# Optimization experiments

Hardware: AMD Instinct MI355X
Metric: run time of the kernel (lower is better)

Reference implementation:

```python
import jax, jax.numpy as jnp
import numpy as np
import math

EMBED_DIM = 512
NUM_HEADS = 8
NUM_EXPERTS = 16
TOP_K = 8
B, T = 2, 1024


def setup_inputs() -> dict:
    key = jax.random.key(0)
    ks = jax.random.split(key, 16)
    d, E = EMBED_DIM, NUM_EXPERTS
    hdim = 4 * d  # expert hidden width
    s = 0.02
    inp = {
        "x": jax.random.normal(ks[0], (B, T, d), jnp.float32),
        # RMSNorm params (init ones, matching torch module)
        "g": jnp.ones((d,), jnp.float32),
        "b": jnp.ones((d,), jnp.float32),
        # attention
        "c_attn_w": jax.random.normal(ks[1], (d, 3 * d), jnp.float32) * s,
        "c_attn_b": jnp.zeros((3 * d,), jnp.float32),
        "alpha": jnp.ones((NUM_HEADS,), jnp.float32),
        "c_proj_w": jax.random.normal(ks[2], (d, d), jnp.float32) * s,
        "c_proj_b": jnp.zeros((d,), jnp.float32),
        # router
        "router_w": jax.random.normal(ks[3], (d, E), jnp.float32) * s,
        "router_b": jnp.zeros((E,), jnp.float32),
        # stacked expert params: Linear(d,4d) -> SwiGLU(4d,4d) -> Linear(4d,d)
        "w_in": jax.random.normal(ks[4], (E, d, hdim), jnp.float32) * s,
        "b_in": jnp.zeros((E, hdim), jnp.float32),
        "w1": jax.random.normal(ks[5], (E, hdim, 2 * hdim), jnp.float32) * s,
        "b1": jnp.zeros((E, 2 * hdim), jnp.float32),
        "w2": jax.random.normal(ks[6], (E, hdim, hdim), jnp.float32) * s,
        "b2": jnp.zeros((E, hdim), jnp.float32),
        "w_out": jax.random.normal(ks[7], (E, hdim, d), jnp.float32) * s,
        "b_out": jnp.zeros((E, d), jnp.float32),
    }
    return inp


def _block(x, g, b, c_attn_w, c_attn_b, alpha, c_proj_w, c_proj_b,
           router_w, router_b, w_in, b_in, w1, b1, w2, b2, w_out, b_out):
    Bb, Tt, C = x.shape
    H = alpha.shape[0]
    hd = C // H
    E = router_b.shape[0]

    # RMSNorm (note: additive b, per original module)
    rms = jnp.sqrt(jnp.mean(x * x, axis=-1, keepdims=True) + 1e-6)
    xn = (x / rms) * g + b

    # QK-normalized causal attention
    qkv = xn @ c_attn_w + c_attn_b                      # [B,T,3C]
    q, k, v = jnp.split(qkv, 3, axis=-1)
    def heads(t):
        return t.reshape(Bb, Tt, H, hd).transpose(0, 2, 1, 3)  # [B,H,T,hd]
    q, k, v = heads(q), heads(k), heads(v)
    eps = 1e-5
    q_hat = q / (jnp.linalg.norm(q, axis=-1, keepdims=True) + eps)
    k_hat = k / (jnp.linalg.norm(k, axis=-1, keepdims=True) + eps)
    factor = (alpha * math.sqrt(hd)).reshape(1, H, 1, 1)
    q_scaled = q_hat * factor
    # SDPA default scale = 1/sqrt(head_dim)
    scores = jnp.einsum("bhqd,bhkd->bhqk", q_scaled, k_hat) / math.sqrt(hd)
    causal = jnp.tril(jnp.ones((Tt, Tt), bool))
    scores = jnp.where(causal, scores, -jnp.inf)
    att = jax.nn.softmax(scores, axis=-1)
    y = jnp.einsum("bhqk,bhkd->bhqd", att, v)
    y = y.transpose(0, 2, 1, 3).reshape(Bb, Tt, C)
    y = y @ c_proj_w + c_proj_b
    x = x + y

    # Router + top-8 normalized gates
    routes = jax.nn.softmax(x @ router_w + router_b, axis=-1)  # [B,T,E]
    probs, idx = jax.lax.top_k(routes, TOP_K)
    probs = probs / jnp.sum(probs, axis=-1, keepdims=True)
    # combine weights per expert: [B,T,E]
    gates = jnp.sum(jax.nn.one_hot(idx, E, dtype=x.dtype) * probs[..., None], axis=2)

    # Dense expert evaluation (faithful math: unselected tokens get zero gate)
    N = Bb * Tt
    xf = x.reshape(N, C)
    gf = gates.reshape(N, E)
    h = jnp.einsum("nd,edf->enf", xf, w_in) + b_in[:, None, :]      # [E,N,4d]
    c = jnp.einsum("enf,efg->eng", h, w1) + b1[:, None, :]          # [E,N,8d]
    a, bb2 = jnp.split(c, 2, axis=-1)
    s = (bb2 * jax.nn.sigmoid(bb2)) * a                              # SwiGLU
    o = jnp.einsum("enf,efg->eng", s, w2) + b2[:, None, :]          # [E,N,4d]
    eo = jnp.einsum("enf,efd->end", o, w_out) + b_out[:, None, :]   # [E,N,d]
    moe = jnp.einsum("end,ne->nd", eo, gf).reshape(Bb, Tt, C)
    return x + moe


def reference(x, g, b, c_attn_w, c_attn_b, alpha, c_proj_w, c_proj_b,
              router_w, router_b, w_in, b_in, w1, b1, w2, b2, w_out, b_out):
    return _block(x, g, b, c_attn_w, c_attn_b, alpha, c_proj_w, c_proj_b,
                  router_w, router_b, w_in, b_in, w1, b1, w2, b2, w_out, b_out)
```

## Files before the change

### kernel.cpp

```cpp
#include <hip/hip_runtime.h>
#include <stdint.h>

#define DEVI __device__ __forceinline__
#define FENCE() asm volatile("" ::: "memory")
#define BAR() do{ FENCE(); __builtin_amdgcn_s_barrier(); FENCE(); }while(0)

typedef short short8 __attribute__((ext_vector_type(8)));
typedef short short4v __attribute__((ext_vector_type(4)));
typedef float f32x4 __attribute__((ext_vector_type(4)));

DEVI float bf2f(unsigned short s){ union{unsigned u; float f;} x; x.u = ((unsigned)s)<<16; return x.f; }
DEVI unsigned short f2bf(float f){ union{float f; unsigned u;} x; x.f=f; unsigned r = x.u + 0x7fff + ((x.u>>16)&1); return (unsigned short)(r>>16); }

DEVI void gload_lds16(const void* g, void* l){
  __builtin_amdgcn_global_load_lds((const __attribute__((address_space(1))) unsigned int*)g,
                                   (__attribute__((address_space(3))) unsigned int*)l, 16, 0, 0);
}

__global__ __launch_bounds__(256)
void prep_all(const float* __restrict__ caw, const float* __restrict__ cpw,
              const float* __restrict__ w_in, const float* __restrict__ w1,
              const float* __restrict__ w2, const float* __restrict__ w_out,
              unsigned short* __restrict__ wT_attn, unsigned short* __restrict__ wT_proj,
              unsigned short* __restrict__ wT_in, unsigned short* __restrict__ wT1p,
              unsigned short* __restrict__ wT_2, unsigned short* __restrict__ wT_out,
              const float* __restrict__ x, const float* __restrict__ gw,
              const float* __restrict__ bw, unsigned short* __restrict__ xn)
{
  __shared__ float tile[8][32][33];
  int bid = blockIdx.x;
  int t = threadIdx.x;
  int tr = t>>3, tc = (t&7)*4;

  const float* src = nullptr; unsigned short* dst = nullptr;
  int K=0, N=0, kb=0, nb0=0;

  if (bid < 96){
    int xb8 = bid % 6, yb = bid / 6;
    src = caw; dst = wT_attn; K=512; N=1536; kb=yb*32; nb0=xb8*256;
  } else if ((bid -= 96) < 32){
    int xb8 = bid % 2, yb = bid / 2;
    src = cpw; dst = wT_proj; K=512; N=512; kb=yb*32; nb0=xb8*256;
  } else if ((bid -= 32) < 2048){
    int z = bid >> 7, r = bid & 127;
    int xb8 = r % 8, yb = r / 8;
    src = w_in + (size_t)z*512*2048; dst = wT_in + (size_t)z*2048*512;
    K=512; N=2048; kb=yb*32; nb0=xb8*256;
  } else if ((bid -= 2048) < 16384){
    int z = bid >> 10, r = bid & 1023;
    int xb8 = r % 16, yb = r / 16;
    const float* s1 = w1 + (size_t)z*2048*4096;
    unsigned short* d1 = wT1p + (size_t)z*4096*2048;
    int k0 = yb*32;
    float4 v[8];
    #pragma unroll
    for (int j=0;j<8;j++){
      int g = xb8*8 + j;
      int srccol = (tc < 16) ? (g*16 + tc) : (2048 + g*16 + (tc-16));
      v[j] = *(const float4*)(s1 + (size_t)(k0+tr)*4096 + srccol);
    }
    #pragma unroll
    for (int j=0;j<8;j++){
      tile[j][tr][tc+0]=v[j].x; tile[j][tr][tc+1]=v[j].y;
      tile[j][tr][tc+2]=v[j].z; tile[j][tr][tc+3]=v[j].w;
    }
    __syncthreads();
    #pragma unroll
    for (int j=0;j<8;j++){
      int np0 = xb8*256 + 32*j;
      short4v ov;
      ov[0] = (short)f2bf(tile[j][tc+0][tr]);
      ov[1] = (short)f2bf(tile[j][tc+1][tr]);
      ov[2] = (short)f2bf(tile[j][tc+2][tr]);
      ov[3] = (short)f2bf(tile[j][tc+3][tr]);
      *(short4v*)(d1 + (size_t)(np0+tr)*2048 + k0 + tc) = ov;
    }
    return;
  } else if ((bid -= 16384) < 8192){
    int z = bid >> 9, r = bid & 511;
    int xb8 = r % 8, yb = r / 8;
    src = w2 + (size_t)z*2048*2048; dst = wT_2 + (size_t)z*2048*2048;
    K=2048; N=2048; kb=yb*32; nb0=xb8*256;
  } else if ((bid -= 8192) < 2048){
    int z = bid >> 7, r = bid & 127;
    int xb8 = r % 2, yb = r / 2;
    src = w_out + (size_t)z*2048*512; dst = wT_out + (size_t)z*512*2048;
    K=2048; N=512; kb=yb*32; nb0=xb8*256;
  } else {
    bid -= 2048;
    int row = bid*4 + (t>>6);
    int lane = t & 63;
    const float* xr = x + (size_t)row*512 + lane*8;
    float4 a = *(const float4*)xr;
    float4 c = *(const float4*)(xr+4);
    float ss = a.x*a.x+a.y*a.y+a.z*a.z+a.w*a.w + c.x*c.x+c.y*c.y+c.z*c.z+c.w*c.w;
    #pragma unroll
    for (int m=1;m<64;m<<=1) ss += __shfl_xor(ss, m);
    float inv = 1.0f / sqrtf(ss*(1.f/512.f) + 1e-6f);
    const float* gr = gw + lane*8; const float* br = bw + lane*8;
    float4 g0=*(const float4*)gr, g1=*(const float4*)(gr+4);
    float4 b0=*(const float4*)br, b1=*(const float4*)(br+4);
    short8 o;
    o[0]=(short)f2bf(a.x*inv*g0.x + b0.x);
    o[1]=(short)f2bf(a.y*inv*g0.y + b0.y);
    o[2]=(short)f2bf(a.z*inv*g0.z + b0.z);
    o[3]=(short)f2bf(a.w*inv*g0.w + b0.w);
    o[4]=(short)f2bf(c.x*inv*g1.x + b1.x);
    o[5]=(short)f2bf(c.y*inv*g1.y + b1.y);
    o[6]=(short)f2bf(c.z*inv*g1.z + b1.z);
    o[7]=(short)f2bf(c.w*inv*g1.w + b1.w);
    *(short8*)(xn + (size_t)row*512 + lane*8) = o;
    return;
  }
  {
    float4 v[8];
    #pragma unroll
    for (int j=0;j<8;j++)
      v[j] = *(const float4*)(src + (size_t)(kb+tr)*N + nb0 + 32*j + tc);
    #pragma unroll
    for (int j=0;j<8;j++){
      tile[j][tr][tc+0]=v[j].x; tile[j][tr][tc+1]=v[j].y;
      tile[j][tr][tc+2]=v[j].z; tile[j][tr][tc+3]=v[j].w;
    }
    __syncthreads();
    #pragma unroll
    for (int j=0;j<8;j++){
      short4v ov;
      ov[0] = (short)f2bf(tile[j][tc+0][tr]);
      ov[1] = (short)f2bf(tile[j][tc+1][tr]);
      ov[2] = (short)f2bf(tile[j][tc+2][tr]);
      ov[3] = (short)f2bf(tile[j][tc+3][tr]);
      *(short4v*)(dst + (size_t)(nb0+32*j+tr)*K + kb + tc) = ov;
    }
  }
}

#define READ_AFR(Q) do{ \
  _Pragma("unroll") \
  for (int m2=0;m2<2;m2++){ \
    int rt = wm*128 + ((Q)*2+m2)*16 + lrow; \
    _Pragma("unroll") \
    for (int kk=0;kk<2;kk++) \
      afr[m2][kk] = *(const short8*)(sA + rt*128 + (((lg+kk*4)^(rt&7))<<4)); \
  } \
}while(0)

#define QUADP(Q) do{ \
  __builtin_amdgcn_s_setprio(1); \
  _Pragma("unroll") \
  for (int m2=0;m2<2;m2++){ \
    _Pragma("unroll") \
    for (int n=0;n<4;n++){ \
      _Pragma("unroll") \
      for (int kk=0;kk<2;kk++) \
        acc[(Q)*2+m2][n] = __builtin_amdgcn_mfma_f32_16x16x32_bf16(afr[m2][kk], bfr[n][kk], acc[(Q)*2+m2][n], 0,0,0); \
    } \
  } \
  __builtin_amdgcn_s_setprio(0); \
}while(0)

template<int EPI>
__global__ __launch_bounds__(512, 2)
void gemmT(const unsigned short* __restrict__ A, const unsigned short* __restrict__ B,
           const float* __restrict__ bias,
           unsigned short* __restrict__ Ch,
           int M, int N, int K,
           const int* __restrict__ off, long long strideBz, long long strideBiasz)
{
  __shared__ char smem[131072];
  int z = blockIdx.z;
  int rowbase = 0, Mz = M;
  if (off){ rowbase = off[z]; Mz = off[z+1] - rowbase; }
  int row0 = blockIdx.y * 256;
  if (row0 >= Mz) return;
  int col0 = blockIdx.x * 256;
  const unsigned short* Ab = A + (size_t)(rowbase + row0) * K;
  const unsigned short* Bb = B + (size_t)z * strideBz + (size_t)col0 * K;
  const float* biasz = bias + (size_t)z * strideBiasz;

  int tid = threadIdx.x;
  int lane = tid & 63, w = tid >> 6;
  int lrow = lane & 15, lg = lane >> 4;
  int wm = w >> 2, wn = w & 3;

  f32x4 acc[8][4];
  #pragma unroll
  for (int i=0;i<8;i++){
    #pragma unroll
    for (int j=0;j<4;j++) acc[i][j] = f32x4{0.f,0.f,0.f,0.f};
  }
  int nkt = K >> 6;
  auto stage = [&](int kt2, int H){
    if (kt2 >= nkt) return;
    char* sl = smem + (kt2 & 1) * 65536 + H * 16384;
    int k0 = kt2 << 6;
    const unsigned short* src = (H < 2) ? Ab : Bb;
    int rbase = (H & 1) * 128;
    #pragma unroll
    for (int i=0;i<2;i++){
      int si = i*512 + tid;
      int r = si >> 3, kb = (si & 7) ^ (r & 7);
      gload_lds16(src + (size_t)(rbase + r)*K + k0 + kb*8, sl + si*16);
    }
  };
  stage(0,0); stage(0,1); stage(0,2); stage(0,3);
  stage(1,2); stage(1,3);
  asm volatile("s_waitcnt vmcnt(4)" ::: "memory");
  BAR();
  for (int kt = 0; kt < nkt; kt++){
    char* sA = smem + (kt & 1) * 65536;
    char* sB = sA + 32768;
    short8 bfr[4][2], afr[2][2];
    #pragma unroll
    for (int n=0;n<4;n++){
      int ct = wn*64 + n*16 + lrow;
      #pragma unroll
      for (int kk=0;kk<2;kk++)
        bfr[n][kk] = *(const short8*)(sB + ct*128 + (((lg+kk*4)^(ct&7))<<4));
    }
    READ_AFR(0);
    stage(kt+1, 0); stage(kt+1, 1);
    BAR();
    QUADP(0);
    BAR();
    READ_AFR(1);
    stage(kt+2, 2);
    BAR();
    QUADP(1);
    BAR();
    READ_AFR(2);
    stage(kt+2, 3);
    BAR();
    QUADP(2);
    BAR();
    READ_AFR(3);
    if (kt + 2 < nkt) { asm volatile("s_waitcnt vmcnt(4)" ::: "memory"); }
    else              { asm volatile("s_waitcnt vmcnt(0)" ::: "memory"); }
    BAR();
    QUADP(3);
    BAR();
  }
  #pragma unroll
  for (int m=0;m<8;m++){
    #pragma unroll
    for (int j=0;j<4;j++){
      int row = row0 + wm*128 + m*16 + lg*4 + j;
      if (row < Mz){
        size_t rg = (size_t)(rowbase + row);
        if constexpr (EPI == 2){
          #pragma unroll
          for (int nf=0;nf<4;nf+=2){
            int pcol = col0 + wn*64 + nf*16;
            int scol = ((pcol>>5)<<4) + lrow;
            float av = acc[m][nf][j]   + biasz[scol];
            float gv = acc[m][nf+1][j] + biasz[2048 + scol];
            float sg = gv / (1.f + __expf(-gv));
            Ch[rg*2048 + scol] = f2bf(av * sg);
          }
        } else {
          #pragma unroll
          for (int n=0;n<4;n++){
            int col = col0 + wn*64 + n*16 + lrow;
            float v = acc[m][n][j] + biasz[col];
            Ch[rg * N + col] = f2bf(v);
          }
        }
      }
    }
  }
}

__global__ __launch_bounds__(256)
void gemm_qkv(const unsigned short* __restrict__ A, const unsigned short* __restrict__ B,
              const float* __restrict__ bias, const float* __restrict__ alpha,
              unsigned short* __restrict__ oq, unsigned short* __restrict__ ok,
              unsigned short* __restrict__ ov, int N, int K)
{
  __shared__ char smem[32768];
  char* smA = smem; char* smB = smem + 16384;
  int row0 = blockIdx.y * 128;
  int col0 = blockIdx.x * 128;
  int t = threadIdx.x, w = t>>6, lane = t&63;
  int lrow = lane&15, lg = lane>>4;
  int wr = w>>1, wc = w&1;

  f32x4 acc[4][4];
  #pragma unroll
  for (int i=0;i<4;i++){
    #pragma unroll
    for (int j=0;j<4;j++) acc[i][j] = f32x4{0.f,0.f,0.f,0.f};
  }
  const size_t Abase = (size_t)row0 * K;
  const size_t Bbase = (size_t)col0 * K;
  int nkt = K >> 6;
  for (int kt=0; kt<nkt; kt++){
    __syncthreads();
    int k0 = kt*64;
    #pragma unroll
    for (int i=0;i<4;i++){
      int s = (i*4 + w)*64 + lane;
      int r = s>>3;
      int kb = (s&7) ^ (r&7);
      gload_lds16(A + Abase + (size_t)r*K + k0 + kb*8, smA + (size_t)(i*4+w)*1024);
      gload_lds16(B + Bbase + (size_t)r*K + k0 + kb*8, smB + (size_t)(i*4+w)*1024);
    }
    __syncthreads();
    #pragma unroll
    for (int ks=0; ks<2; ks++){
      short8 af[4], bf[4];
      int kbb = lg + ks*4;
      #pragma unroll
      for (int m=0;m<4;m++){
        int rt = wr*64 + m*16 + lrow;
        af[m] = *(const short8*)(smA + rt*128 + ((kbb ^ (rt&7))<<4));
      }
      #pragma unroll
      for (int n=0;n<4;n++){
        int rt = wc*64 + n*16 + lrow;
        bf[n] = *(const short8*)(smB + rt*128 + ((kbb ^ (rt&7))<<4));
      }
      #pragma unroll
      for (int m=0;m<4;m++){
        #pragma unroll
        for (int n=0;n<4;n++)
          acc[m][n] = __builtin_amdgcn_mfma_f32_16x16x32_bf16(af[m], bf[n], acc[m][n], 0,0,0);
      }
    }
  }
  int tcol = col0 + wc*64;
  int type = tcol >> 9;
  int hd = (tcol >> 6) & 7;
  float al = alpha[hd];
  #pragma unroll
  for (int m=0;m<4;m++){
    #pragma unroll
    for (int j=0;j<4;j++){
      int row = row0 + wr*64 + m*16 + lg*4 + j;
      float v4[4]; float ss = 0.f;
      #pragma unroll
      for (int n=0;n<4;n++){
        v4[n] = acc[m][n][j] + bias[tcol + n*16 + lrow];
        ss += v4[n]*v4[n];
      }
      ss += __shfl_xor(ss,1); ss += __shfl_xor(ss,2);
      ss += __shfl_xor(ss,4); ss += __shfl_xor(ss,8);
      int b = row >> 10, tt = row & 1023;
      size_t hb = ((size_t)(b*8+hd))*65536;
      if (type == 0){
        float sc = al / (sqrtf(ss) + 1e-5f);
        #pragma unroll
        for (int n=0;n<4;n++)
          oq[hb + (size_t)tt*64 + n*16 + lrow] = f2bf(v4[n]*sc);
      } else if (type == 1){
        float sc = 1.f / (sqrtf(ss) + 1e-5f);
        #pragma unroll
        for (int n=0;n<4;n++)
          ok[hb + (size_t)tt*64 + n*16 + lrow] = f2bf(v4[n]*sc);
      } else {
        #pragma unroll
        for (int n=0;n<4;n++)
          ov[((size_t)(b*8+hd)*64 + n*16 + lrow)*1024 + tt] = f2bf(v4[n]);
      }
    }
  }
}

__global__ __launch_bounds__(256)
void gemm_proj(const unsigned short* __restrict__ A, const unsigned short* __restrict__ B,
               const float* __restrict__ bias,
               float* __restrict__ Cf, unsigned short* __restrict__ Ch,
               const float* __restrict__ resid, int M, int N, int K)
{
  __shared__ char smem[32768];
  char* smA = smem; char* smB = smem + 16384;
  int row0 = blockIdx.y * 128;
  int col0 = blockIdx.x * 128;
  int t = threadIdx.x, w = t>>6, lane = t&63;
  int lrow = lane&15, lg = lane>>4;
  int wr = w>>1, wc = w&1;

  f32x4 acc[4][4];
  #pragma unroll
  for (int i=0;i<4;i++){
    #pragma unroll
    for (int j=0;j<4;j++) acc[i][j] = f32x4{0.f,0.f,0.f,0.f};
  }
  const size_t Abase = (size_t)row0 * K;
  const size_t Bbase = (size_t)col0 * K;
  int nkt = K >> 6;
  for (int kt=0; kt<nkt; kt++){
    __syncthreads();
    int k0 = kt*64;
    #pragma unroll
    for (int i=0;i<4;i++){
      int s = (i*4 + w)*64 + lane;
      int r = s>>3;
      int kb = (s&7) ^ (r&7);
      gload_lds16(A + Abase + (size_t)r*K + k0 + kb*8, smA + (size_t)(i*4+w)*1024);
      gload_lds16(B + Bbase + (size_t)r*K + k0 + kb*8, smB + (size_t)(i*4+w)*1024);
    }
    __syncthreads();
    #pragma unroll
    for (int ks=0; ks<2; ks++){
      short8 af[4], bf[4];
      int kbb = lg + ks*4;
      #pragma unroll
      for (int m=0;m<4;m++){
        int rt = wr*64 + m*16 + lrow;
        af[m] = *(const short8*)(smA + rt*128 + ((kbb ^ (rt&7))<<4));
      }
      #pragma unroll
      for (int n=0;n<4;n++){
        int rt = wc*64 + n*16 + lrow;
        bf[n] = *(const short8*)(smB + rt*128 + ((kbb ^ (rt&7))<<4));
      }
      #pragma unroll
      for (int m=0;m<4;m++){
        #pragma unroll
        for (int n=0;n<4;n++)
          acc[m][n] = __builtin_amdgcn_mfma_f32_16x16x32_bf16(af[m], bf[n], acc[m][n], 0,0,0);
      }
    }
  }
  #pragma unroll
  for (int m=0;m<4;m++){
    int rloc = wr*64 + m*16 + lg*4;
    #pragma unroll
    for (int j=0;j<4;j++){
      int row = row0 + rloc + j;
      size_t rg = (size_t)row;
      #pragma unroll
      for (int n=0;n<4;n++){
        int col = col0 + wc*64 + n*16 + lrow;
        float v = acc[m][n][j] + bias[col];
        size_t idx = rg * N + col;
        v += resid[idx];
        Cf[idx] = v;
        Ch[idx] = f2bf(v);
      }
    }
  }
}

__global__ __launch_bounds__(256)
void attn_k(const unsigned short* __restrict__ q_s, const unsigned short* __restrict__ k_hat,
            const unsigned short* __restrict__ v_t, unsigned short* __restrict__ y)
{
  __shared__ char sm[51200];
  char* smK = sm + 18432;
  char* smV = sm + 34816;
  int qt = blockIdx.x, bh = blockIdx.y;
  int b = bh>>3, h = bh&7;
  int t = threadIdx.x, w = t>>6, lane = t&63;
  int lrow = lane&15, lg = lane>>4;
  int q0 = qt*64;
  const size_t hQK = (size_t)bh*1024*64;
  const size_t hV  = (size_t)bh*64*1024;

  #pragma unroll
  for (int i=0;i<2;i++){
    int si = i*256 + t;
    int r = si>>3, kb = (si&7)^(r&7);
    gload_lds16(q_s + hQK + (size_t)(q0+r)*64 + kb*8, sm + (size_t)si*16);
  }
  __syncthreads();
  short8 qf[2];
  #pragma unroll
  for (int ks=0;ks<2;ks++){
    int rt = w*16 + lrow;
    int kbb = lg + ks*4;
    qf[ks] = *(const short8*)(sm + rt*128 + ((kbb^(rt&7))<<4));
  }
  f32x4 oacc[4];
  #pragma unroll
  for (int j=0;j<4;j++) oacc[j] = f32x4{0.f,0.f,0.f,0.f};
  float mrun[4], lrun[4];
  #pragma unroll
  for (int j=0;j<4;j++){ mrun[j] = -1e30f; lrun[j] = 0.f; }
  char* Pw = sm + w*2304;

  int ktmax = (q0 + 63) >> 7;
  for (int kt=0; kt<=ktmax; kt++){
    __syncthreads();
    int t0 = kt*128;
    #pragma unroll
    for (int i=0;i<4;i++){
      int s = (i*4+w)*64 + lane;
      int r = s>>3, kb = (s&7)^(r&7);
      gload_lds16(k_hat + hQK + (size_t)(t0+r)*64 + kb*8, smK + (size_t)(i*4+w)*1024);
    }
    #pragma unroll
    for (int i=0;i<4;i++){
      int s = (i*4+w)*64 + lane;
      int d = s>>4, kb2 = s&15;
      int kb = kb2 ^ (d&7);
      gload_lds16(v_t + hV + (size_t)d*1024 + t0 + kb*8, smV + (size_t)(i*4+w)*1024);
    }
    __syncthreads();

    f32x4 sacc[8];
    #pragma unroll
    for (int j=0;j<8;j++) sacc[j] = f32x4{0.f,0.f,0.f,0.f};
    #pragma unroll
    for (int ks=0;ks<2;ks++){
      short8 kf[8];
      int kbb = lg + ks*4;
      #pragma unroll
      for (int nf=0;nf<8;nf++){
        int rt = nf*16+lrow;
        kf[nf] = *(const short8*)(smK + rt*128 + ((kbb^(rt&7))<<4));
      }
      #pragma unroll
      for (int nf=0;nf<8;nf++)
        sacc[nf] = __builtin_amdgcn_mfma_f32_16x16x32_bf16(qf[ks], kf[nf], sacc[nf], 0,0,0);
    }
    if (kt == ktmax){
      #pragma unroll
      for (int nf=0;nf<8;nf++){
        #pragma unroll
        for (int j=0;j<4;j++){
          int qi = q0 + w*16 + lg*4 + j;
          int ki = t0 + nf*16 + lrow;
          if (ki > qi) sacc[nf][j] = -1e30f;
        }
      }
    }
    #pragma unroll
    for (int j=0;j<4;j++){
      float mx = sacc[0][j];
      #pragma unroll
      for (int nf=1;nf<8;nf++) mx = fmaxf(mx, sacc[nf][j]);
      #pragma unroll
      for (int m=1;m<16;m<<=1) mx = fmaxf(mx, __shfl_xor(mx, m));
      float mnew = fmaxf(mrun[j], mx);
      float sc = __expf(mrun[j] - mnew);
      float rs = 0.f;
      #pragma unroll
      for (int nf=0;nf<8;nf++){
        float p = __expf(sacc[nf][j] - mnew);
        sacc[nf][j] = p; rs += p;
      }
      #pragma unroll
      for (int m=1;m<16;m<<=1) rs += __shfl_xor(rs, m);
      lrun[j] = lrun[j]*sc + rs;
      mrun[j] = mnew;
      #pragma unroll
      for (int n2=0;n2<4;n2++) oacc[n2][j] *= sc;
    }
    #pragma unroll
    for (int half=0; half<2; half++){
      #pragma unroll
      for (int nfh=0;nfh<4;nfh++){
        int nf = half*4 + nfh;
        #pragma unroll
        for (int j=0;j<4;j++){
          int row = lg*4 + j;
          int col = nfh*16 + lrow;
          *(unsigned short*)(Pw + (row*72 + col)*2) = f2bf(sacc[nf][j]);
        }
      }
      #pragma unroll
      for (int k2=0;k2<2;k2++){
        int ks2 = half*2 + k2;
        short8 pf, vf[4];
        pf = *(const short8*)(Pw + lrow*144 + lg*16 + k2*64);
        #pragma unroll
        for (int n2=0;n2<4;n2++){
          int d = n2*16+lrow;
          int kbb2 = lg + ks2*4;
          vf[n2] = *(const short8*)(smV + d*256 + ((kbb2^(d&7))<<4));
        }
        #pragma unroll
        for (int n2=0;n2<4;n2++)
          oacc[n2] = __builtin_amdgcn_mfma_f32_16x16x32_bf16(pf, vf[n2], oacc[n2], 0,0,0);
      }
    }
  }
  #pragma unroll
  for (int n2=0;n2<4;n2++){
    #pragma unroll
    for (int j=0;j<4;j++){
      float v = oacc[n2][j] / lrun[j];
      int qi = q0 + w*16 + lg*4 + j;
      int d = n2*16 + lrow;
      y[((size_t)(b*1024+qi))*512 + h*64 + d] = f2bf(v);
    }
  }
}

__global__ __launch_bounds__(256)
void router_topk(const float* __restrict__ x2f, const float* __restrict__ rw,
                 const float* __restrict__ rb, float* __restrict__ gates)
{
  int tkn = blockIdx.x*4 + (threadIdx.x>>6);
  int lane = threadIdx.x & 63;
  int e = lane & 15, p = lane >> 4;
  const float* xr = x2f + (size_t)tkn*512;
  float part = 0.f;
  for (int d = p*128; d < p*128+128; d++)
    part += xr[d] * rw[d*16 + e];
  part += __shfl_xor(part, 16);
  part += __shfl_xor(part, 32);
  float logit = part + rb[e];
  float mx = logit;
  #pragma unroll
  for (int m=1;m<16;m<<=1) mx = fmaxf(mx, __shfl_xor(mx, m));
  float ex = __expf(logit - mx);
  float sm = ex;
  #pragma unroll
  for (int m=1;m<16;m<<=1) sm += __shfl_xor(sm, m);
  float prob = ex / sm;
  bool taken = false;
  float ssum = 0.f;
  #pragma unroll
  for (int r=0;r<8;r++){
    float cv = taken ? -1.f : prob;
    int ci = e;
    #pragma unroll
    for (int m=1;m<16;m<<=1){
      float ov = __shfl_xor(cv, m);
      int oi = __shfl_xor(ci, m);
      if (ov > cv || (ov == cv && oi < ci)){ cv = ov; ci = oi; }
    }
    if (e == ci) taken = true;
    ssum += cv;
  }
  if (lane < 16)
    gates[(size_t)tkn*16 + e] = taken ? prob / ssum : 0.f;
}

__global__ void listbuild(const float* __restrict__ gates, int* __restrict__ list,
                          int* __restrict__ slot, int* __restrict__ cnt)
{
  int e = blockIdx.x;
  int tid = threadIdx.x, w = tid>>6, lane = tid&63;
  __shared__ int sbase;
  __shared__ int wsum[4];
  if (tid==0) sbase = 0;
  __syncthreads();
  for (int c=0;c<8;c++){
    int tk = c*256 + tid;
    bool flag = gates[(size_t)tk*16 + e] > 0.f;
    unsigned long long bal = __ballot(flag);
    if (lane==0) wsum[w] = (int)__popcll(bal);
    __syncthreads();
    int wpref = 0;
    for (int i=0;i<w;i++) wpref += wsum[i];
    int tot = wsum[0]+wsum[1]+wsum[2]+wsum[3];
    int lpref = (int)__popcll(bal & ((1ull<<lane)-1ull));
    if (flag){
      int pos = sbase + wpref + lpref;
      list[e*2048 + pos] = tk;
      slot[(size_t)tk*16 + e] = pos;
    }
    __syncthreads();
    if (tid==0) sbase += tot;
    __syncthreads();
  }
  if (tid==0) cnt[e] = sbase;
}

__global__ void prefix_off(const int* __restrict__ cnt, int* __restrict__ off){
  if (threadIdx.x==0 && blockIdx.x==0){
    int a=0;
    for (int e=0;e<16;e++){ off[e]=a; a+=cnt[e]; }
    off[16]=a;
  }
}

__global__ __launch_bounds__(256)
void gather_rows(const unsigned short* __restrict__ x2h, const int* __restrict__ list,
                 const int* __restrict__ cnt, const int* __restrict__ off,
                 unsigned short* __restrict__ xe)
{
  int e = blockIdx.y;
  int s = blockIdx.x*4 + (threadIdx.x>>6);
  if (s >= cnt[e]) return;
  int lane = threadIdx.x & 63;
  int tk = list[e*2048 + s];
  *(short8*)(xe + ((size_t)(off[e]+s))*512 + lane*8) =
      *(const short8*)(x2h + (size_t)tk*512 + lane*8);
}

__global__ __launch_bounds__(256)
void combine_k(const float* __restrict__ x2f, const unsigned short* __restrict__ eo,
               const float* __restrict__ gates, const int* __restrict__ slot,
               const int* __restrict__ off, float* __restrict__ out)
{
  int tkn = blockIdx.x;
  __shared__ float gs[16];
  __shared__ int rws[16];
  int tid = threadIdx.x;
  if (tid < 16){
    float g = gates[(size_t)tkn*16 + tid];
    gs[tid] = g;
    rws[tid] = (g > 0.f) ? (off[tid] + slot[(size_t)tkn*16 + tid]) : 0;
  }
  __syncthreads();
  for (int d = tid; d < 512; d += 256){
    float v = x2f[(size_t)tkn*512 + d];
    #pragma unroll
    for (int e=0;e<16;e++){
      float g = gs[e];
      if (g > 0.f) v += g * bf2f(eo[(size_t)rws[e]*512 + d]);
    }
    out[(size_t)tkn*512 + d] = v;
  }
}

extern "C" void kernel_launch(void* const* d_in, const int* in_sizes, int n_in,
                              void* d_out, int out_size, void* d_ws, size_t ws_size,
                              hipStream_t stream) {
  (void)in_sizes; (void)n_in; (void)out_size; (void)ws_size;
  const float* x    = (const float*)d_in[0];
  const float* gw   = (const float*)d_in[1];
  const float* bw   = (const float*)d_in[2];
  const float* caw  = (const float*)d_in[3];
  const float* cab  = (const float*)d_in[4];
  const float* alpha= (const float*)d_in[5];
  const float* cpw  = (const float*)d_in[6];
  const float* cpb  = (const float*)d_in[7];
  const float* rw   = (const float*)d_in[8];
  const float* rb   = (const float*)d_in[9];
  const float* w_in = (const float*)d_in[10];
  const float* b_in = (const float*)d_in[11];
  const float* w1   = (const float*)d_in[12];
  const float* b1   = (const float*)d_in[13];
  const float* w2   = (const float*)d_in[14];
  const float* b2   = (const float*)d_in[15];
  const float* w_out= (const float*)d_in[16];
  const float* b_out= (const float*)d_in[17];

  char* ws = (char*)d_ws;
  size_t o = 0;
  auto alloc = [&](size_t bytes)->char*{
    char* p = ws + o;
    o += (bytes + 255) & ~(size_t)255;
    return p;
  };
  const size_t PADROWS = 16896;
  unsigned short* wT_attn = (unsigned short*)alloc(1536ull*512*2);
  unsigned short* wT_proj = (unsigned short*)alloc(512ull*512*2);
  unsigned short* wT_in   = (unsigned short*)alloc(16ull*2048*512*2);
  unsigned short* wT1p    = (unsigned short*)alloc(16ull*4096*2048*2);
  unsigned short* wT_2    = (unsigned short*)alloc(16ull*2048*2048*2);
  unsigned short* wT_out  = (unsigned short*)alloc(16ull*512*2048*2);
  unsigned short* xn      = (unsigned short*)alloc(2048ull*512*2);
  unsigned short* q_s     = (unsigned short*)alloc(2048ull*512*2);
  unsigned short* k_hat   = (unsigned short*)alloc(2048ull*512*2);
  unsigned short* v_t     = (unsigned short*)alloc(2048ull*512*2);
  unsigned short* ybuf    = (unsigned short*)alloc(2048ull*512*2);
  float*          x2f     = (float*)alloc(2048ull*512*4);
  unsigned short* x2h     = (unsigned short*)alloc(2048ull*512*2);
  float*          gates   = (float*)alloc(2048ull*16*4);
  int*            slot    = (int*)alloc(2048ull*16*4);
  int*            list    = (int*)alloc(16ull*2048*4);
  int*            cnt     = (int*)alloc(64);
  int*            off     = (int*)alloc(256);
  unsigned short* xe      = (unsigned short*)alloc(PADROWS*512*2);
  unsigned short* hbuf    = (unsigned short*)alloc(PADROWS*2048*2);
  unsigned short* sbuf    = (unsigned short*)alloc(PADROWS*2048*2);
  unsigned short* eobuf   = xe;
  unsigned short* obuf    = hbuf;

  dim3 blk(256);
  dim3 blk5(512);
  prep_all<<<29312, blk, 0, stream>>>(caw, cpw, w_in, w1, w2, w_out,
                                      wT_attn, wT_proj, wT_in, wT1p, wT_2, wT_out,
                                      x, gw, bw, xn);

  gemm_qkv<<<dim3(12, 16), blk, 0, stream>>>(xn, wT_attn, cab, alpha,
                                             q_s, k_hat, v_t, 1536, 512);
  attn_k<<<dim3(16,16), blk, 0, stream>>>(q_s, k_hat, v_t, ybuf);
  gemm_proj<<<dim3(4,16,1), blk, 0, stream>>>(ybuf, wT_proj, cpb, x2f, x2h, x, 2048, 512, 512);
  router_topk<<<512, blk, 0, stream>>>(x2f, rw, rb, gates);
  listbuild<<<16, blk, 0, stream>>>(gates, list, slot, cnt);
  prefix_off<<<1, 64, 0, stream>>>(cnt, off);
  gather_rows<<<dim3(512,16), blk, 0, stream>>>(x2h, list, cnt, off, xe);

  gemmT<1><<<dim3(8,8,16), blk5, 0, stream>>>(xe, wT_in, b_in, hbuf,
                                              0, 2048, 512, off, 2048ll*512, 2048);
  gemmT<2><<<dim3(16,8,16), blk5, 0, stream>>>(hbuf, wT1p, b1, sbuf,
                                               0, 4096, 2048, off, 4096ll*2048, 4096);
  gemmT<1><<<dim3(8,8,16), blk5, 0, stream>>>(sbuf, wT_2, b2, obuf,
                                              0, 2048, 2048, off, 2048ll*2048, 2048);
  gemmT<1><<<dim3(2,8,16), blk5, 0, stream>>>(obuf, wT_out, b_out, eobuf,
                                              0, 512, 2048, off, 512ll*2048, 512);
  combine_k<<<2048, blk, 0, stream>>>(x2f, eobuf, gates, slot, off, (float*)d_out);
}
```

Baseline: 1.002 ms.

## Replace pipelined 256x256 expert GEMM with simple 128x128 single-buffer kernel

The expert GEMMs move from a 512-thread kernel with 256x256 tiles, double-buffered LDS and staged prefetch interleaved with MFMA quads to a 256-thread kernel with 128x128 tiles and one LDS buffer that loads then computes each k-step. Smaller tiles cut padding waste on experts with few rows and raise block count and occupancy. The cost is no global-load/compute overlap, two syncthreads per k-step, and less operand reuse per block, which increases global traffic.

Result: slower. 1.056 ms (+5.3%).

```diff
diff --git a/kernel.cpp b/kernel.cpp
--- a/kernel.cpp
+++ b/kernel.cpp
@@ -135,122 +135,81 @@
   }
 }
 
-#define READ_AFR(Q) do{ \
-  _Pragma("unroll") \
-  for (int m2=0;m2<2;m2++){ \
-    int rt = wm*128 + ((Q)*2+m2)*16 + lrow; \
-    _Pragma("unroll") \
-    for (int kk=0;kk<2;kk++) \
-      afr[m2][kk] = *(const short8*)(sA + rt*128 + (((lg+kk*4)^(rt&7))<<4)); \
-  } \
-}while(0)
-
-#define QUADP(Q) do{ \
-  __builtin_amdgcn_s_setprio(1); \
-  _Pragma("unroll") \
-  for (int m2=0;m2<2;m2++){ \
-    _Pragma("unroll") \
-    for (int n=0;n<4;n++){ \
-      _Pragma("unroll") \
-      for (int kk=0;kk<2;kk++) \
-        acc[(Q)*2+m2][n] = __builtin_amdgcn_mfma_f32_16x16x32_bf16(afr[m2][kk], bfr[n][kk], acc[(Q)*2+m2][n], 0,0,0); \
-    } \
-  } \
-  __builtin_amdgcn_s_setprio(0); \
-}while(0)
-
 template<int EPI>
-__global__ __launch_bounds__(512, 2)
-void gemmT(const unsigned short* __restrict__ A, const unsigned short* __restrict__ B,
+__global__ __launch_bounds__(256)
+void gemmE(const unsigned short* __restrict__ A, const unsigned short* __restrict__ B,
            const float* __restrict__ bias,
            unsigned short* __restrict__ Ch,
-           int M, int N, int K,
+           int N, int K,
            const int* __restrict__ off, long long strideBz, long long strideBiasz)
 {
-  __shared__ char smem[131072];
+  __shared__ char smem[32768];
+  char* smA = smem; char* smB = smem + 16384;
   int z = blockIdx.z;
-  int rowbase = 0, Mz = M;
-  if (off){ rowbase = off[z]; Mz = off[z+1] - rowbase; }
-  int row0 = blockIdx.y * 256;
+  int rowbase = off[z], Mz = off[z+1] - rowbase;
+  int row0 = blockIdx.y * 128;
   if (row0 >= Mz) return;
-  int col0 = blockIdx.x * 256;
+  int col0 = blockIdx.x * 128;
   const unsigned short* Ab = A + (size_t)(rowbase + row0) * K;
   const unsigned short* Bb = B + (size_t)z * strideBz + (size_t)col0 * K;
   const float* biasz = bias + (size_t)z * strideBiasz;
 
-  int tid = threadIdx.x;
-  int lane = tid & 63, w = tid >> 6;
-  int lrow = lane & 15, lg = lane >> 4;
-  int wm = w >> 2, wn = w & 3;
-
-  f32x4 acc[8][4];
-  #pragma unroll
-  for (int i=0;i<8;i++){
+  int t = threadIdx.x, w = t>>6, lane = t&63;
+  int lrow = lane&15, lg = lane>>4;
+  int wr = w>>1, wc = w&1;
+
+  f32x4 acc[4][4];
+  #pragma unroll
+  for (int i=0;i<4;i++){
     #pragma unroll
     for (int j=0;j<4;j++) acc[i][j] = f32x4{0.f,0.f,0.f,0.f};
   }
   int nkt = K >> 6;
-  auto stage = [&](int kt2, int H){
-    if (kt2 >= nkt) return;
-    char* sl = smem + (kt2 & 1) * 65536 + H * 16384;
-    int k0 = kt2 << 6;
-    const unsigned short* src = (H < 2) ? Ab : Bb;
-    int rbase = (H & 1) * 128;
-    #pragma unroll
-    for (int i=0;i<2;i++){
-      int si = i*512 + tid;
-      int r = si >> 3, kb = (si & 7) ^ (r & 7);
-      gload_lds16(src + (size_t)(rbase + r)*K + k0 + kb*8, sl + si*16);
-    }
-  };
-  stage(0,0); stage(0,1); stage(0,2); stage(0,3);
-  stage(1,2); stage(1,3);
-  asm volatile("s_waitcnt vmcnt(4)" ::: "memory");
-  BAR();
-  for (int kt = 0; kt < nkt; kt++){
-    char* sA = smem + (kt & 1) * 65536;
-    char* sB = sA + 32768;
-    short8 bfr[4][2], afr[2][2];
-    #pragma unroll
-    for (int n=0;n<4;n++){
-      int ct = wn*64 + n*16 + lrow;
-      #pragma unroll
-      for (int kk=0;kk<2;kk++)
-        bfr[n][kk] = *(const short8*)(sB + ct*128 + (((lg+kk*4)^(ct&7))<<4));
-    }
-    READ_AFR(0);
-    stage(kt+1, 0); stage(kt+1, 1);
-    BAR();
-    QUADP(0);
-    BAR();
-    READ_AFR(1);
-    stage(kt+2, 2);
-    BAR();
-    QUADP(1);
-    BAR();
-    READ_AFR(2);
-    stage(kt+2, 3);
-    BAR();
-    QUADP(2);
-    BAR();
-    READ_AFR(3);
-    if (kt + 2 < nkt) { asm volatile("s_waitcnt vmcnt(4)" ::: "memory"); }
-    else              { asm volatile("s_waitcnt vmcnt(0)" ::: "memory"); }
-    BAR();
-    QUADP(3);
-    BAR();
-  }
-  #pragma unroll
-  for (int m=0;m<8;m++){
+  for (int kt=0; kt<nkt; kt++){
+    __syncthreads();
+    int k0 = kt*64;
+    #pragma unroll
+    for (int i=0;i<4;i++){
+      int s = (i*4 + w)*64 + lane;
+      int r = s>>3;
+      int kb = (s&7) ^ (r&7);
+      gload_lds16(Ab + (size_t)r*K + k0 + kb*8, smA + (size_t)(i*4+w)*1024);
+      gload_lds16(Bb + (size_t)r*K + k0 + kb*8, smB + (size_t)(i*4+w)*1024);
+    }
+    __syncthreads();
+    #pragma unroll
+    for (int ks=0; ks<2; ks++){
+      short8 af[4], bf[4];
+      int kbb = lg + ks*4;
+      #pragma unroll
+      for (int m=0;m<4;m++){
+        int rt = wr*64 + m*16 + lrow;
+        af[m] = *(const short8*)(smA + rt*128 + ((kbb ^ (rt&7))<<4));
+      }
+      #pragma unroll
+      for (int n=0;n<4;n++){
+        int rt = wc*64 + n*16 + lrow;
+        bf[n] = *(const short8*)(smB + rt*128 + ((kbb ^ (rt&7))<<4));
+      }
+      #pragma unroll
+      for (int m=0;m<4;m++){
+        #pragma unroll
+        for (int n=0;n<4;n++)
+          acc[m][n] = __builtin_amdgcn_mfma_f32_16x16x32_bf16(af[m], bf[n], acc[m][n], 0,0,0);
+      }
+    }
+  }
+  #pragma unroll
+  for (int m=0;m<4;m++){
     #pragma unroll
     for (int j=0;j<4;j++){
-      int row = row0 + wm*128 + m*16 + lg*4 + j;
+      int row = row0 + wr*64 + m*16 + lg*4 + j;
       if (row < Mz){
         size_t rg = (size_t)(rowbase + row);
         if constexpr (EPI == 2){
           #pragma unroll
           for (int nf=0;nf<4;nf+=2){
-            int pcol = col0 + wn*64 + nf*16;
+            int pcol = col0 + wc*64 + nf*16;
             int scol = ((pcol>>5)<<4) + lrow;
             float av = acc[m][nf][j]   + biasz[scol];
             float gv = acc[m][nf+1][j] + biasz[2048 + scol];
@@ -260,7 +219,7 @@
         } else {
           #pragma unroll
           for (int n=0;n<4;n++){
-            int col = col0 + wn*64 + n*16 + lrow;
+            int col = col0 + wc*64 + n*16 + lrow;
             float v = acc[m][n][j] + biasz[col];
             Ch[rg * N + col] = f2bf(v);
           }
@@ -764,7 +723,6 @@
   unsigned short* obuf    = hbuf;
 
   dim3 blk(256);
-  dim3 blk5(512);
   prep_all<<<29312, blk, 0, stream>>>(caw, cpw, w_in, w1, w2, w_out,
                                       wT_attn, wT_proj, wT_in, wT1p, wT_2, wT_out,
                                       x, gw, bw, xn);
@@ -778,13 +736,13 @@
   prefix_off<<<1, 64, 0, stream>>>(cnt, off);
   gather_rows<<<dim3(512,16), blk, 0, stream>>>(x2h, list, cnt, off, xe);
 
-  gemmT<1><<<dim3(8,8,16), blk5, 0, stream>>>(xe, wT_in, b_in, hbuf,
-                                              0, 2048, 512, off, 2048ll*512, 2048);
-  gemmT<2><<<dim3(16,8,16), blk5, 0, stream>>>(hbuf, wT1p, b1, sbuf,
-                                               0, 4096, 2048, off, 4096ll*2048, 4096);
-  gemmT<1><<<dim3(8,8,16), blk5, 0, stream>>>(sbuf, wT_2, b2, obuf,
-                                              0, 2048, 2048, off, 2048ll*2048, 2048);
-  gemmT<1><<<dim3(2,8,16), blk5, 0, stream>>>(obuf, wT_out, b_out, eobuf,
-                                              0, 512, 2048, off, 512ll*2048, 512);
+  gemmE<1><<<dim3(16,16,16), blk, 0, stream>>>(xe, wT_in, b_in, hbuf,
+                                               2048, 512, off, 2048ll*512, 2048);
+  gemmE<2><<<dim3(32,16,16), blk, 0, stream>>>(hbuf, wT1p, b1, sbuf,
+                                               4096, 2048, off, 4096ll*2048, 4096);
+  gemmE<1><<<dim3(16,16,16), blk, 0, stream>>>(sbuf, wT_2, b2, obuf,
+                                               2048, 2048, off, 2048ll*2048, 2048);
+  gemmE<1><<<dim3(4,16,16), blk, 0, stream>>>(obuf, wT_out, b_out, eobuf,
+                                              512, 2048, off, 512ll*2048, 512);
   combine_k<<<2048, blk, 0, stream>>>(x2f, eobuf, gates, slot, off, (float*)d_out);
 }
```
